# Performance work log

Measured on AMD Instinct MI355X. Metric: run time of the kernel, lower is better.

The kernel has to match this reference:

```python
import jax, jax.numpy as jnp
import numpy as np

SCALE = 4
A = -0.75


def _bicubic_kernels():
    # cubic convolution coefficient matrix (Keys, a=-0.75), matching the torch module
    cubic = np.array([[0.0, A, -2.0 * A, A],
                      [1.0, 0.0, -(A + 3.0), A + 2.0],
                      [0.0, -A, 2.0 * A + 3.0, -(A + 2.0)],
                      [0.0, 0.0, A, -A]], dtype=np.float32)
    rows = []
    for d in range(SCALE):
        sv = np.float32(d) / np.float32(SCALE)
        rows.append(cubic @ np.array([1.0, sv, sv ** 2, sv ** 3], dtype=np.float32))
    return jnp.asarray(np.stack(rows))  # [s, 4] tap weights per sub-pixel phase


def setup_inputs() -> dict:
    key = jax.random.key(0)
    x = jax.random.normal(key, (16, 3, 256, 256), dtype=jnp.float32)
    return {"x": x, "kernels": _bicubic_kernels()}


def reference(x, kernels):
    n, c, h, w = x.shape
    s = kernels.shape[0]  # scale factor
    # replicate pad: (left=1, right=2, top=1, bottom=2)
    xp = jnp.pad(x, ((0, 0), (0, 0), (1, 2), (1, 2)), mode='edge')  # [n,c,h+3,w+3]
    wp = w + 3
    # vertical pass: 4-tap weighted sum over height, producing s phases per row
    win = jnp.stack([xp[:, :, j:j + h, :] for j in range(4)], axis=-1)  # [n,c,h,w+3,4]
    out = jnp.einsum('nchwj,kj->nchkw', win, kernels)  # [n,c,h,s,w+3]
    out = out.reshape(n, c, h * s, wp)  # interleave phases along height
    # horizontal pass: 4-tap weighted sum over width, s phases per column
    win = jnp.stack([out[:, :, :, j:j + w] for j in range(4)], axis=-1)  # [n,c,h*s,w,4]
    out = jnp.einsum('nchwj,kj->nchwk', win, kernels)  # [n,c,h*s,w,s]
    return out.reshape(n, c, h * s, w * s)
```

## Files before the change

### kernel.cpp

```cpp
#include <hip/hip_runtime.h>

#define H  256
#define W  256
#define S  4
#define OH (H * S)
#define OW (W * S)

typedef float f32x4 __attribute__((ext_vector_type(4)));

#define K1A -0.10546875f
#define K1B  0.87890625f
#define K1C  0.26171875f
#define K1D -0.03515625f
#define K2A -0.09375f
#define K2B  0.59375f
#define K2C  0.59375f
#define K2D -0.09375f

__global__ __launch_bounds__(256, 8) void bicubic_up4(
    const float* __restrict__ x, const float* __restrict__ kern,
    float* __restrict__ out)
{
    __shared__ float lds[7][W];

    const int iw  = threadIdx.x;
    const int ihb = blockIdx.x * 4;
    const int nc  = blockIdx.y;

    const float* __restrict__ xp = x + (size_t)nc * (H * W);

#pragma unroll
    for (int t = 0; t < 7; ++t) {
        int r = ihb - 1 + t;
        r = r < 0 ? 0 : (r > H - 1 ? H - 1 : r);
        lds[t][iw] = xp[r * W + iw];
    }
    __syncthreads();

    const int c0 = max(iw - 1, 0);
    const int c2 = min(iw + 1, W - 1);
    const int c3 = min(iw + 2, W - 1);

    float hb[7][4];
#pragma unroll
    for (int t = 0; t < 7; ++t) {
        const float a = lds[t][c0];
        const float b = lds[t][iw];
        const float c = lds[t][c2];
        const float d = lds[t][c3];
        hb[t][0] = b;
        hb[t][1] = K1A * a + K1B * b + K1C * c + K1D * d;
        hb[t][2] = K2A * a + K2B * b + K2C * c + K2D * d;
        hb[t][3] = K1D * a + K1C * b + K1B * c + K1A * d;
    }

    float* __restrict__ obase =
        out + ((size_t)nc * OH + (size_t)ihb * S) * OW + (size_t)iw * S;

#pragma unroll
    for (int q = 0; q < 4; ++q) {
#pragma unroll
        for (int kv = 0; kv < 4; ++kv) {
            f32x4 o;
            if (kv == 0) {
                o.x = hb[q + 1][0];
                o.y = hb[q + 1][1];
                o.z = hb[q + 1][2];
                o.w = hb[q + 1][3];
            } else {
                const float w0 = (kv == 1) ? K1A : (kv == 2) ? K2A : K1D;
                const float w1 = (kv == 1) ? K1B : (kv == 2) ? K2B : K1C;
                const float w2 = (kv == 1) ? K1C : (kv == 2) ? K2C : K1B;
                const float w3 = (kv == 1) ? K1D : (kv == 2) ? K2D : K1A;
                o.x = hb[q][0]*w0 + hb[q+1][0]*w1 + hb[q+2][0]*w2 + hb[q+3][0]*w3;
                o.y = hb[q][1]*w0 + hb[q+1][1]*w1 + hb[q+2][1]*w2 + hb[q+3][1]*w3;
                o.z = hb[q][2]*w0 + hb[q+1][2]*w1 + hb[q+2][2]*w2 + hb[q+3][2]*w3;
                o.w = hb[q][3]*w0 + hb[q+1][3]*w1 + hb[q+2][3]*w2 + hb[q+3][3]*w3;
            }
            __builtin_nontemporal_store(
                o, reinterpret_cast<f32x4*>(obase + ((size_t)(q * S + kv)) * OW));
        }
    }
}

extern "C" void kernel_launch(void* const* d_in, const int* in_sizes, int n_in,
                              void* d_out, int out_size, void* d_ws, size_t ws_size,
                              hipStream_t stream) {
    const float* x    = (const float*)d_in[0];
    const float* kern = (const float*)d_in[1];
    float* out        = (float*)d_out;
    (void)kern;

    dim3 grid(H / 4, 16 * 3);
    dim3 block(256);
    bicubic_up4<<<grid, block, 0, stream>>>(x, kern, out);
}
```

Baseline: 219.6 us.

## Stream rows through a register ring buffer and drop LDS staging

```diff
diff --git a/kernel.cpp b/kernel.cpp
--- a/kernel.cpp
+++ b/kernel.cpp
@@ -5,8 +5,10 @@
 #define S  4
 #define OH (H * S)
 #define OW (W * S)
+#define SLAB 8
 
 typedef float f32x4 __attribute__((ext_vector_type(4)));
+typedef f32x4 __attribute__((aligned(4))) f32x4_u;
 
 #define K1A -0.10546875f
 #define K1B  0.87890625f
@@ -21,66 +23,85 @@
     const float* __restrict__ x, const float* __restrict__ kern,
     float* __restrict__ out)
 {
-    __shared__ float lds[7][W];
-
     const int iw  = threadIdx.x;
-    const int ihb = blockIdx.x * 4;
+    const int ihb = blockIdx.x * SLAB;
     const int nc  = blockIdx.y;
 
     const float* __restrict__ xp = x + (size_t)nc * (H * W);
 
-#pragma unroll
-    for (int t = 0; t < 7; ++t) {
-        int r = ihb - 1 + t;
-        r = r < 0 ? 0 : (r > H - 1 ? H - 1 : r);
-        lds[t][iw] = xp[r * W + iw];
-    }
-    __syncthreads();
-
+    const bool interior = (iw >= 1) && (iw <= W - 3);
     const int c0 = max(iw - 1, 0);
     const int c2 = min(iw + 1, W - 1);
     const int c3 = min(iw + 2, W - 1);
 
-    float hb[7][4];
+    float wbuf[4][4];
+
+#define FETCH(RR, A, B, C, D)                                                  \
+    {                                                                          \
+        int r_ = (RR);                                                         \
+        r_ = r_ < 0 ? 0 : (r_ > H - 1 ? H - 1 : r_);                           \
+        const float* __restrict__ row_ = xp + r_ * W;                          \
+        if (interior) {                                                        \
+            f32x4 v_ = *reinterpret_cast<const f32x4_u*>(row_ + (iw - 1));     \
+            A = v_.x; B = v_.y; C = v_.z; D = v_.w;                            \
+        } else {                                                               \
+            A = row_[c0]; B = row_[iw]; C = row_[c2]; D = row_[c3];            \
+        }                                                                      \
+    }
+
+#define HFILT(A, B, C, D, DST)                                                 \
+    {                                                                          \
+        DST[0] = (B);                                                          \
+        DST[1] = K1A*(A) + K1B*(B) + K1C*(C) + K1D*(D);                        \
+        DST[2] = K2A*(A) + K2B*(B) + K2C*(C) + K2D*(D);                        \
+        DST[3] = K1D*(A) + K1C*(B) + K1B*(C) + K1A*(D);                        \
+    }
+
 #pragma unroll
-    for (int t = 0; t < 7; ++t) {
-        const float a = lds[t][c0];
-        const float b = lds[t][iw];
-        const float c = lds[t][c2];
-        const float d = lds[t][c3];
-        hb[t][0] = b;
-        hb[t][1] = K1A * a + K1B * b + K1C * c + K1D * d;
-        hb[t][2] = K2A * a + K2B * b + K2C * c + K2D * d;
-        hb[t][3] = K1D * a + K1C * b + K1B * c + K1A * d;
+    for (int m = 0; m < 4; ++m) {
+        float a, b, c, d;
+        FETCH(ihb - 1 + m, a, b, c, d);
+        HFILT(a, b, c, d, wbuf[m]);
     }
 
     float* __restrict__ obase =
         out + ((size_t)nc * OH + (size_t)ihb * S) * OW + (size_t)iw * S;
 
+#define R(J, COL) wbuf[(q + (J)) & 3][COL]
+
 #pragma unroll
-    for (int q = 0; q < 4; ++q) {
-#pragma unroll
-        for (int kv = 0; kv < 4; ++kv) {
-            f32x4 o;
-            if (kv == 0) {
-                o.x = hb[q + 1][0];
-                o.y = hb[q + 1][1];
-                o.z = hb[q + 1][2];
-                o.w = hb[q + 1][3];
-            } else {
-                const float w0 = (kv == 1) ? K1A : (kv == 2) ? K2A : K1D;
-                const float w1 = (kv == 1) ? K1B : (kv == 2) ? K2B : K1C;
-                const float w2 = (kv == 1) ? K1C : (kv == 2) ? K2C : K1B;
-                const float w3 = (kv == 1) ? K1D : (kv == 2) ? K2D : K1A;
-                o.x = hb[q][0]*w0 + hb[q+1][0]*w1 + hb[q+2][0]*w2 + hb[q+3][0]*w3;
-                o.y = hb[q][1]*w0 + hb[q+1][1]*w1 + hb[q+2][1]*w2 + hb[q+3][1]*w3;
-                o.z = hb[q][2]*w0 + hb[q+1][2]*w1 + hb[q+2][2]*w2 + hb[q+3][2]*w3;
-                o.w = hb[q][3]*w0 + hb[q+1][3]*w1 + hb[q+2][3]*w2 + hb[q+3][3]*w3;
-            }
-            __builtin_nontemporal_store(
-                o, reinterpret_cast<f32x4*>(obase + ((size_t)(q * S + kv)) * OW));
-        }
+    for (int q = 0; q < SLAB; ++q) {
+        float na, nb, ncc, nd;
+        if (q < SLAB - 1) FETCH(ihb + q + 3, na, nb, ncc, nd);
+
+        f32x4 o;
+        o.x = R(1,0); o.y = R(1,1); o.z = R(1,2); o.w = R(1,3);
+        __builtin_nontemporal_store(
+            o, reinterpret_cast<f32x4*>(obase + (size_t)(q * S + 0) * OW));
+        o.x = K1A*R(0,0) + K1B*R(1,0) + K1C*R(2,0) + K1D*R(3,0);
+        o.y = K1A*R(0,1) + K1B*R(1,1) + K1C*R(2,1) + K1D*R(3,1);
+        o.z = K1A*R(0,2) + K1B*R(1,2) + K1C*R(2,2) + K1D*R(3,2);
+        o.w = K1A*R(0,3) + K1B*R(1,3) + K1C*R(2,3) + K1D*R(3,3);
+        __builtin_nontemporal_store(
+            o, reinterpret_cast<f32x4*>(obase + (size_t)(q * S + 1) * OW));
+        o.x = K2A*R(0,0) + K2B*R(1,0) + K2C*R(2,0) + K2D*R(3,0);
+        o.y = K2A*R(0,1) + K2B*R(1,1) + K2C*R(2,1) + K2D*R(3,1);
+        o.z = K2A*R(0,2) + K2B*R(1,2) + K2C*R(2,2) + K2D*R(3,2);
+        o.w = K2A*R(0,3) + K2B*R(1,3) + K2C*R(2,3) + K2D*R(3,3);
+        __builtin_nontemporal_store(
+            o, reinterpret_cast<f32x4*>(obase + (size_t)(q * S + 2) * OW));
+        o.x = K1D*R(0,0) + K1C*R(1,0) + K1B*R(2,0) + K1A*R(3,0);
+        o.y = K1D*R(0,1) + K1C*R(1,1) + K1B*R(2,1) + K1A*R(3,1);
+        o.z = K1D*R(0,2) + K1C*R(1,2) + K1B*R(2,2) + K1A*R(3,2);
+        o.w = K1D*R(0,3) + K1C*R(1,3) + K1B*R(2,3) + K1A*R(3,3);
+        __builtin_nontemporal_store(
+            o, reinterpret_cast<f32x4*>(obase + (size_t)(q * S + 3) * OW));
+
+        if (q < SLAB - 1) HFILT(na, nb, ncc, nd, wbuf[q & 3]);
     }
+#undef R
+#undef HFILT
+#undef FETCH
 }
 
 extern "C" void kernel_launch(void* const* d_in, const int* in_sizes, int n_in,
@@ -91,7 +112,7 @@
     float* out        = (float*)d_out;
     (void)kern;
 
-    dim3 grid(H / 4, 16 * 3);
+    dim3 grid(H / SLAB, 16 * 3);
     dim3 block(256);
     bicubic_up4<<<grid, block, 0, stream>>>(x, kern, out);
 }
```

Result: slower. 239.4 us (+9.1%).
